# Optimization experiments

Hardware: AMD Instinct MI355X
Metric: run time of the kernel (lower is better)

The kernel has to match this reference:

```python
import jax, jax.numpy as jnp
import numpy as np

D_X, D_H, N_I = 1024, 64, 16  # model dim, per-head dim (d_q=d_k=d_v), heads
BSZ, SEQ = 2, 2048


def _linear(x, W, b):
    return x @ W.T + b


def setup_inputs() -> dict:
    key = jax.random.key(0)
    ks = jax.random.split(key, 16)
    s_in = 1.0 / np.sqrt(D_X)
    s_hd = 1.0 / np.sqrt(N_I * D_H)
    return {
        "query": jax.random.normal(ks[0], (BSZ, SEQ, D_X), jnp.float32),
        "key": jax.random.normal(ks[1], (BSZ, SEQ, D_X), jnp.float32),
        "value": jax.random.normal(ks[2], (BSZ, SEQ, D_X), jnp.float32),
        "Wq": jax.random.normal(ks[3], (N_I * D_H, D_X), jnp.float32) * s_in,
        "bq": jnp.zeros((N_I * D_H,), jnp.float32),
        "Wk": jax.random.normal(ks[4], (N_I * D_H, D_X), jnp.float32) * s_in,
        "bk": jnp.zeros((N_I * D_H,), jnp.float32),
        "Wv": jax.random.normal(ks[5], (N_I * D_H, D_X), jnp.float32) * s_in,
        "bv": jnp.zeros((N_I * D_H,), jnp.float32),
        "Wxv": jax.random.normal(ks[6], (N_I * D_H, D_X), jnp.float32) * s_in,
        "bxv": jnp.zeros((N_I * D_H,), jnp.float32),
        "Wxo": jax.random.normal(ks[7], (D_X, N_I * D_H), jnp.float32) * s_hd,
        "bxo": jnp.zeros((D_X,), jnp.float32),
        "Wmo": jax.random.normal(ks[8], (D_X, N_I * D_H), jnp.float32) * s_hd,
        "bmo": jnp.zeros((D_X,), jnp.float32),
    }


def reference(query, key, value, Wq, bq, Wk, bk, Wv, bv, Wxv, bxv, Wxo, bxo, Wmo, bmo):
    bsz, seq, _ = query.shape

    def heads(x):  # (b, s, n_I*d) -> (b, h, s, d)
        return x.reshape(bsz, seq, N_I, D_H).transpose(0, 2, 1, 3)

    Q = heads(_linear(query, Wq, bq))
    K = heads(_linear(key, Wk, bk))
    V = heads(_linear(value, Wv, bv))

    dot = jnp.einsum('bhid,bhjd->bhij', Q, K) / jnp.sqrt(jnp.float32(D_H))
    attention = jax.nn.softmax(dot, axis=-1)  # dropout p=0 (eval)

    # use_xv=True: replace K with xV = W_xv(key) for the k_bar aggregation
    xV = heads(_linear(key, Wxv, bxv))

    k_bar = jnp.einsum('bhjd,bhij->bhid', xV, attention)
    v_bar = jnp.einsum('bhjd,bhij->bhid', V, attention)

    def merge(x):  # (b, h, s, d) -> (b, s, h*d)
        return x.transpose(0, 2, 1, 3).reshape(bsz, seq, N_I * D_H)

    x = _linear(merge(k_bar), Wxo, bxo)
    m = _linear(merge(v_bar), Wmo, bmo)
    return (x, m)
```

## Files before the change

kernel.cpp:

```cpp
#include <hip/hip_runtime.h>
#include <math.h>

typedef __bf16 bf16;
typedef __bf16 bf16x2 __attribute__((ext_vector_type(2)));
typedef __bf16 bf16x4 __attribute__((ext_vector_type(4)));
typedef __bf16 bf16x8 __attribute__((ext_vector_type(8)));
typedef float f32x4 __attribute__((ext_vector_type(4)));

#define SEQ 2048
#define DH 64
#define DX 1024
#define NH 16
#define LP 72

static __device__ __forceinline__ f32x4 mfma16(bf16x8 a, bf16x8 b, f32x4 c) {
    return __builtin_amdgcn_mfma_f32_16x16x32_bf16(a, b, c, 0, 0, 0);
}
static __device__ __forceinline__ bf16x8 cvt8(const float* __restrict__ p) {
    f32x4 a = *(const f32x4*)p;
    f32x4 b = *(const f32x4*)(p + 4);
    bf16x8 r;
    #pragma unroll
    for (int j = 0; j < 4; ++j) { r[j] = (bf16)a[j]; r[4 + j] = (bf16)b[j]; }
    return r;
}

#define GL16(gp, lp) __builtin_amdgcn_global_load_lds( \
    (const __attribute__((address_space(1))) void*)(gp), \
    (__attribute__((address_space(3))) void*)(lp), 16, 0, 0)


__global__ __launch_bounds__(256) void cvt_all(
    const float* __restrict__ q, const float* __restrict__ k,
    const float* __restrict__ v,
    const float* __restrict__ w0, const float* __restrict__ w1,
    const float* __restrict__ w2, const float* __restrict__ w3,
    const float* __restrict__ w4, const float* __restrict__ w5,
    bf16* __restrict__ out)
{
    const size_t i = (size_t)blockIdx.x * 2048 + threadIdx.x * 8;
    const int seg = (int)(i >> 20);
    const float* s;
    size_t off;
    if (seg < 4)       { s = q; off = i; }
    else if (seg < 8)  { s = k; off = i - (4ull << 20); }
    else if (seg < 12) { s = v; off = i - (8ull << 20); }
    else {
        const float* ww[6] = {w0, w1, w2, w3, w4, w5};
        s = ww[seg - 12]; off = i - ((size_t)seg << 20);
    }
    *(bf16x8*)(out + i) = cvt8(s + off);
}

struct G4 {
    const bf16* X[4]; const bf16* W[4]; const float* B[4];
    bf16* Yb[4]; float* Yf[4]; int xmode[4]; int ymode[4];
};
__global__ __launch_bounds__(256) void gemm_fused(G4 a)
{
    __shared__ __align__(16) bf16 As[128 * 64];
    __shared__ __align__(16) bf16 Bs[128 * 64];

    const int z = blockIdx.z;
    const bf16* __restrict__ X = a.X[z];
    const bf16* __restrict__ W = a.W[z];
    const int xmode = a.xmode[z], ymode = a.ymode[z];

    const int tid  = threadIdx.x;
    const int wave = tid >> 6;
    const int lane = tid & 63;
    const int l16  = lane & 15;
    const int quad = lane >> 4;
    const int m0 = blockIdx.y * 128;
    const int n0 = blockIdx.x * 128;
    const int mw = (wave >> 1) * 64;
    const int nw = (wave & 1) * 64;

    const int srow = wave * 32 + (lane >> 3);
    const int scol = (lane & 7) * 8;

    f32x4 acc[4][4];
    #pragma unroll
    for (int i = 0; i < 4; ++i)
        #pragma unroll
        for (int j = 0; j < 4; ++j) acc[i][j] = (f32x4){0.f,0.f,0.f,0.f};

    for (int kb = 0; kb < DX / 64; ++kb) {
        __syncthreads();
        if (xmode == 0) {
            const bf16* ga = X + (size_t)(m0 + srow) * DX + kb * 64 + scol;
            #pragma unroll
            for (int j = 0; j < 4; ++j)
                GL16(ga + (size_t)j * 8 * DX, &As[(wave * 32 + j * 8) * 64]);
        } else {
            #pragma unroll
            for (int j = 0; j < 4; ++j) {
                const int m = m0 + srow + j * 8;
                const int b = m >> 11, s = m & 2047;
                GL16(X + ((size_t)(b * NH + kb) * SEQ + s) * DH + scol,
                     &As[(wave * 32 + j * 8) * 64]);
            }
        }
        {
            const bf16* gb = W + (size_t)(n0 + srow) * DX + kb * 64 + scol;
            #pragma unroll
            for (int j = 0; j < 4; ++j)
                GL16(gb + (size_t)j * 8 * DX, &Bs[(wave * 32 + j * 8) * 64]);
        }
        __syncthreads();

        #pragma unroll
        for (int ks = 0; ks < 2; ++ks) {
            bf16x8 af[4], bfr[4];
            #pragma unroll
            for (int mf = 0; mf < 4; ++mf)
                af[mf] = *(const bf16x8*)&As[(mw + mf * 16 + l16) * 64 + ks * 32 + quad * 8];
            #pragma unroll
            for (int nf = 0; nf < 4; ++nf)
                bfr[nf] = *(const bf16x8*)&Bs[(nw + nf * 16 + l16) * 64 + ks * 32 + quad * 8];
            #pragma unroll
            for (int mf = 0; mf < 4; ++mf)
                #pragma unroll
                for (int nf = 0; nf < 4; ++nf)
                    acc[mf][nf] = mfma16(af[mf], bfr[nf], acc[mf][nf]);
        }
    }

    #pragma unroll
    for (int nf = 0; nf < 4; ++nf) {
        const int col = n0 + nw + nf * 16 + l16;
        const float bvv = a.B[z][col];
        #pragma unroll
        for (int mf = 0; mf < 4; ++mf) {
            #pragma unroll
            for (int r = 0; r < 4; ++r) {
                const int row = m0 + mw + mf * 16 + quad * 4 + r;
                const float vv = acc[mf][nf][r] + bvv;
                if (ymode == 0) {
                    const int b = row >> 11, s = row & 2047;
                    const int h = col >> 6, d = col & 63;
                    a.Yb[z][((size_t)(b * NH + h) * SEQ + s) * DH + d] = (bf16)vv;
                } else {
                    a.Yf[z][(size_t)row * DX + col] = vv;
                }
            }
        }
    }
}

__global__ __launch_bounds__(256) void attn_fast(
    bf16* __restrict__ Q, const bf16* __restrict__ K,
    const bf16* __restrict__ V, const bf16* __restrict__ xV,
    bf16* __restrict__ VB)
{
    __shared__ __align__(16) bf16 Ks[2][64 * 64];
    __shared__ __align__(16) bf16 Vt [64 * LP];
    __shared__ __align__(16) bf16 xVt[64 * LP];
    __shared__ __align__(16) bf16 Pl[4][32 * LP];

    const int tid  = threadIdx.x;
    const int wave = tid >> 6;
    const int lane = tid & 63;
    const int l16  = lane & 15;
    const int quad = lane >> 4;
    const size_t hb = ((size_t)blockIdx.z * NH + blockIdx.y) * SEQ * DH;
    const int q0 = blockIdx.x * 128 + wave * 32;

    bf16x8 qf[2][2];
    #pragma unroll
    for (int mf = 0; mf < 2; ++mf)
        #pragma unroll
        for (int ks = 0; ks < 2; ++ks)
            qf[mf][ks] = *(const bf16x8*)(Q + hb + (size_t)(q0 + mf*16 + l16) * DH + ks*32 + quad*8);

    bf16x8 one8;
    #pragma unroll
    for (int j = 0; j < 8; ++j) one8[j] = (bf16)1.0f;

    f32x4 ov[2][4], oxv[2][4];
    f32x4 rsa[2];
    rsa[0] = (f32x4){0.f,0.f,0.f,0.f};
    rsa[1] = (f32x4){0.f,0.f,0.f,0.f};
    #pragma unroll
    for (int mf = 0; mf < 2; ++mf)
        #pragma unroll
        for (int c = 0; c < 4; ++c) {
            ov[mf][c]  = (f32x4){0.f,0.f,0.f,0.f};
            oxv[mf][c] = (f32x4){0.f,0.f,0.f,0.f};
        }

    const int krow = lane >> 3;
    const int kch  = (lane & 7) ^ krow;
    const int vkp = (tid & 31) * 2;
    const int vd0 = (tid >> 5) * 8;
    const float SCL = 0.125f * 1.4426950408889634f;

    bf16x8 pv0, pv1, px0, px1;
    {
        const bf16* kg = K + hb + (size_t)(wave*16 + krow) * DH + kch*8;
        GL16(kg,            &Ks[0][(wave*16 + 0) * 64]);
        GL16(kg + 8 * DH,   &Ks[0][(wave*16 + 8) * 64]);
        const size_t g0 = hb + (size_t)vkp * DH + vd0;
        pv0 = *(const bf16x8*)(V  + g0);
        pv1 = *(const bf16x8*)(V  + g0 + DH);
        px0 = *(const bf16x8*)(xV + g0);
        px1 = *(const bf16x8*)(xV + g0 + DH);
    }

    int c = 0;
    for (int kt = 0; kt < SEQ; kt += 64) {
        #pragma unroll
        for (int j = 0; j < 8; ++j) {
            *(bf16x2*)&Vt [(vd0 + j) * LP + vkp] = (bf16x2){pv0[j], pv1[j]};
            *(bf16x2*)&xVt[(vd0 + j) * LP + vkp] = (bf16x2){px0[j], px1[j]};
        }
        if (kt + 64 < SEQ) {
            const bf16* kg = K + hb + (size_t)(kt + 64 + wave*16 + krow) * DH + kch*8;
            GL16(kg,          &Ks[c ^ 1][(wave*16 + 0) * 64]);
            GL16(kg + 8 * DH, &Ks[c ^ 1][(wave*16 + 8) * 64]);
            const size_t g0 = hb + (size_t)(kt + 64 + vkp) * DH + vd0;
            pv0 = *(const bf16x8*)(V  + g0);
            pv1 = *(const bf16x8*)(V  + g0 + DH);
            px0 = *(const bf16x8*)(xV + g0);
            px1 = *(const bf16x8*)(xV + g0 + DH);
        }
        __asm__ volatile("s_waitcnt lgkmcnt(0)" ::: "memory");
        __builtin_amdgcn_s_barrier();
        __asm__ volatile("s_waitcnt vmcnt(6)" ::: "memory");
        __builtin_amdgcn_sched_barrier(0);

        f32x4 sf[4][2];
        #pragma unroll
        for (int mf = 0; mf < 4; ++mf)
            #pragma unroll
            for (int nf = 0; nf < 2; ++nf) sf[mf][nf] = (f32x4){0.f,0.f,0.f,0.f};
        __builtin_amdgcn_s_setprio(1);
        #pragma unroll
        for (int ks = 0; ks < 2; ++ks)
            #pragma unroll
            for (int mf = 0; mf < 4; ++mf) {
                bf16x8 kf = *(const bf16x8*)&Ks[c][(mf*16 + l16) * 64 +
                                                   (((ks*4 + quad) ^ (l16 & 7)) * 8)];
                sf[mf][0] = mfma16(kf, qf[0][ks], sf[mf][0]);
                sf[mf][1] = mfma16(kf, qf[1][ks], sf[mf][1]);
            }
        __builtin_amdgcn_s_setprio(0);

        #pragma unroll
        for (int nf = 0; nf < 2; ++nf)
            #pragma unroll
            for (int mf = 0; mf < 4; ++mf) {
                float p0 = __builtin_amdgcn_exp2f(sf[mf][nf][0] * SCL);
                float p1 = __builtin_amdgcn_exp2f(sf[mf][nf][1] * SCL);
                float p2 = __builtin_amdgcn_exp2f(sf[mf][nf][2] * SCL);
                float p3 = __builtin_amdgcn_exp2f(sf[mf][nf][3] * SCL);
                *(bf16x4*)&Pl[wave][(nf * 16 + l16) * LP + mf * 16 + quad * 4] =
                    (bf16x4){(bf16)p0, (bf16)p1, (bf16)p2, (bf16)p3};
            }
        __asm__ volatile("s_waitcnt lgkmcnt(0)" ::: "memory");
        __builtin_amdgcn_sched_barrier(0);

        __builtin_amdgcn_s_setprio(1);
        #pragma unroll
        for (int ks = 0; ks < 2; ++ks) {
            bf16x8 pa0 = *(const bf16x8*)&Pl[wave][(l16)      * LP + ks * 32 + quad * 8];
            bf16x8 pa1 = *(const bf16x8*)&Pl[wave][(16 + l16) * LP + ks * 32 + quad * 8];
            rsa[0] = mfma16(pa0, one8, rsa[0]);
            rsa[1] = mfma16(pa1, one8, rsa[1]);
            #pragma unroll
            for (int cc = 0; cc < 4; ++cc) {
                bf16x8 bv = *(const bf16x8*)&Vt [(cc * 16 + l16) * LP + ks * 32 + quad * 8];
                ov[0][cc]  = mfma16(pa0, bv, ov[0][cc]);
                ov[1][cc]  = mfma16(pa1, bv, ov[1][cc]);
                bf16x8 bx = *(const bf16x8*)&xVt[(cc * 16 + l16) * LP + ks * 32 + quad * 8];
                oxv[0][cc] = mfma16(pa0, bx, oxv[0][cc]);
                oxv[1][cc] = mfma16(pa1, bx, oxv[1][cc]);
            }
        }
        __builtin_amdgcn_s_setprio(0);

        __builtin_amdgcn_sched_barrier(0);
        __builtin_amdgcn_s_barrier();
        c ^= 1;
    }

    #pragma unroll
    for (int mf = 0; mf < 2; ++mf)
        #pragma unroll
        for (int r = 0; r < 4; ++r) {
            const int qrow = mf * 16 + quad * 4 + r;
            const float inv = 1.0f / rsa[mf][r];
            const size_t base = hb + (size_t)(q0 + qrow) * DH;
            #pragma unroll
            for (int cc = 0; cc < 4; ++cc) {
                const int d = cc * 16 + l16;
                Q [base + d] = (bf16)(oxv[mf][cc][r] * inv);
                VB[base + d] = (bf16)(ov[mf][cc][r]  * inv);
            }
        }
}


__global__ __launch_bounds__(256) void proj_gemm(
    const void* __restrict__ Xv, const float* __restrict__ W,
    const float* __restrict__ bias, void* __restrict__ Yv,
    int in_kind, int out_mode)
{
    __shared__ __align__(16) bf16 As[64 * LP];
    __shared__ __align__(16) bf16 Bs[128 * LP];
    const int tid  = threadIdx.x;
    const int wave = tid >> 6;
    const int lane = tid & 63;
    const int l16  = lane & 15;
    const int quad = lane >> 4;
    const int m0 = blockIdx.y * 64;
    const int n0 = blockIdx.x * 128;
    const int m_w = (wave >> 1) * 32;
    const int n_w = (wave & 1) * 64;
    const int ar = tid >> 2, ac = (tid & 3) * 16;
    const int br = tid >> 1, bc = (tid & 1) * 32;

    f32x4 acc[2][4];
    #pragma unroll
    for (int i = 0; i < 2; ++i)
        #pragma unroll
        for (int j = 0; j < 4; ++j) acc[i][j] = (f32x4){0.f,0.f,0.f,0.f};

    for (int kb = 0; kb < DX / 64; ++kb) {
        __syncthreads();
        if (in_kind == 0) {
            const float* xp = (const float*)Xv + (size_t)(m0 + ar) * DX + kb * 64 + ac;
            *(bf16x8*)&As[ar * LP + ac]     = cvt8(xp);
            *(bf16x8*)&As[ar * LP + ac + 8] = cvt8(xp + 8);
        } else {
            const bf16* xp = (const bf16*)Xv + ((size_t)kb * SEQ + (m0 + ar)) * DH + ac;
            *(bf16x8*)&As[ar * LP + ac]     = *(const bf16x8*)xp;
            *(bf16x8*)&As[ar * LP + ac + 8] = *(const bf16x8*)(xp + 8);
        }
        {
            const float* wp = W + (size_t)(n0 + br) * DX + kb * 64 + bc;
            #pragma unroll
            for (int g = 0; g < 4; ++g)
                *(bf16x8*)&Bs[br * LP + bc + g * 8] = cvt8(wp + g * 8);
        }
        __syncthreads();
        #pragma unroll
        for (int ks = 0; ks < 2; ++ks) {
            bf16x8 a0 = *(const bf16x8*)&As[(m_w + l16)      * LP + ks * 32 + quad * 8];
            bf16x8 a1 = *(const bf16x8*)&As[(m_w + 16 + l16) * LP + ks * 32 + quad * 8];
            #pragma unroll
            for (int nf = 0; nf < 4; ++nf) {
                bf16x8 b = *(const bf16x8*)&Bs[(n_w + nf * 16 + l16) * LP + ks * 32 + quad * 8];
                acc[0][nf] = mfma16(a0, b, acc[0][nf]);
                acc[1][nf] = mfma16(a1, b, acc[1][nf]);
            }
        }
    }
    #pragma unroll
    for (int mf = 0; mf < 2; ++mf)
        #pragma unroll
        for (int nf = 0; nf < 4; ++nf) {
            const int col = n0 + n_w + nf * 16 + l16;
            const float bvv = bias[col];
            #pragma unroll
            for (int r = 0; r < 4; ++r) {
                const int row = m0 + m_w + mf * 16 + quad * 4 + r;
                float v = acc[mf][nf][r] + bvv;
                if (out_mode == 0) {
                    int h = col >> 6, d = col & 63;
                    ((bf16*)Yv)[((size_t)h * SEQ + row) * DH + d] = (bf16)v;
                } else {
                    ((float*)Yv)[(size_t)row * DX + col] = v;
                }
            }
        }
}

__global__ __launch_bounds__(256) void attn_dual(
    bf16* __restrict__ Q, const bf16* __restrict__ K,
    const bf16* __restrict__ V, const bf16* __restrict__ xV,
    bf16* __restrict__ vb)
{
    __shared__ __align__(16) bf16 Ks [64 * LP];
    __shared__ __align__(16) bf16 Vt [64 * LP];
    __shared__ __align__(16) bf16 xVt[64 * LP];
    __shared__ __align__(16) bf16 Pl[4][32 * LP];
    const int tid  = threadIdx.x;
    const int h    = blockIdx.y;
    const int qt   = blockIdx.x;
    const int wave = tid >> 6;
    const int lane = tid & 63;
    const int l16  = lane & 15;
    const int quad = lane >> 4;
    const size_t hb = (size_t)h * SEQ * DH;
    const int q0 = qt * 128 + wave * 32;

    bf16x8 qf[2][2];
    #pragma unroll
    for (int mf = 0; mf < 2; ++mf)
        #pragma unroll
        for (int ks = 0; ks < 2; ++ks)
            qf[mf][ks] = *(const bf16x8*)(Q + hb + (size_t)(q0 + mf*16 + l16) * DH + ks*32 + quad*8);

    float mr[2][4], lr[2][4];
    f32x4 ov[2][4], oxv[2][4];
    #pragma unroll
    for (int mf = 0; mf < 2; ++mf)
        #pragma unroll
        for (int r = 0; r < 4; ++r) { mr[mf][r] = -1e30f; lr[mf][r] = 0.f; }
    #pragma unroll
    for (int mf = 0; mf < 2; ++mf)
        #pragma unroll
        for (int c = 0; c < 4; ++c) {
            ov[mf][c]  = (f32x4){0.f,0.f,0.f,0.f};
            oxv[mf][c] = (f32x4){0.f,0.f,0.f,0.f};
        }
    const int sr = tid >> 2, sc = (tid & 3) * 16;
    const int vkp = (tid & 31) * 2;
    const int vd0 = (tid >> 5) * 8;
    const float SCL = 0.125f * 1.4426950408889634f;

    for (int kt = 0; kt < SEQ; kt += 64) {
        __syncthreads();
        {
            const bf16* kpt = K + hb + (size_t)(kt + sr) * DH + sc;
            *(bf16x8*)&Ks[sr * LP + sc]     = *(const bf16x8*)kpt;
            *(bf16x8*)&Ks[sr * LP + sc + 8] = *(const bf16x8*)(kpt + 8);
            const size_t g0 = hb + (size_t)(kt + vkp) * DH + vd0;
            bf16x8 v0 = *(const bf16x8*)(V + g0);
            bf16x8 v1 = *(const bf16x8*)(V + g0 + DH);
            bf16x8 x0 = *(const bf16x8*)(xV + g0);
            bf16x8 x1 = *(const bf16x8*)(xV + g0 + DH);
            #pragma unroll
            for (int j = 0; j < 8; ++j) {
                *(bf16x2*)&Vt [(vd0 + j) * LP + vkp] = (bf16x2){v0[j], v1[j]};
                *(bf16x2*)&xVt[(vd0 + j) * LP + vkp] = (bf16x2){x0[j], x1[j]};
            }
        }
        __syncthreads();
        f32x4 sf[2][4];
        #pragma unroll
        for (int mf = 0; mf < 2; ++mf)
            #pragma unroll
            for (int nf = 0; nf < 4; ++nf) sf[mf][nf] = (f32x4){0.f,0.f,0.f,0.f};
        #pragma unroll
        for (int ks = 0; ks < 2; ++ks)
            #pragma unroll
            for (int nf = 0; nf < 4; ++nf) {
                bf16x8 bk = *(const bf16x8*)&Ks[(nf * 16 + l16) * LP + ks * 32 + quad * 8];
                sf[0][nf] = mfma16(qf[0][ks], bk, sf[0][nf]);
                sf[1][nf] = mfma16(qf[1][ks], bk, sf[1][nf]);
            }
        float mx[2][4], rs[2][4], alpha[2][4];
        #pragma unroll
        for (int mf = 0; mf < 2; ++mf)
            #pragma unroll
            for (int r = 0; r < 4; ++r) {
                float aa = fmaxf(sf[mf][0][r], sf[mf][1][r]);
                float bb = fmaxf(sf[mf][2][r], sf[mf][3][r]);
                mx[mf][r] = fmaxf(aa, bb) * SCL;
            }
        #pragma unroll
        for (int off = 1; off < 16; off <<= 1)
            #pragma unroll
            for (int mf = 0; mf < 2; ++mf)
                #pragma unroll
                for (int r = 0; r < 4; ++r)
                    mx[mf][r] = fmaxf(mx[mf][r], __shfl_xor(mx[mf][r], off, 64));
        #pragma unroll
        for (int mf = 0; mf < 2; ++mf)
            #pragma unroll
            for (int r = 0; r < 4; ++r) {
                float mnew = fmaxf(mr[mf][r], mx[mf][r]);
                alpha[mf][r] = exp2f(mr[mf][r] - mnew);
                mr[mf][r] = mnew;
            }
        bf16* pw = &Pl[wave][0];
        #pragma unroll
        for (int mf = 0; mf < 2; ++mf)
            #pragma unroll
            for (int r = 0; r < 4; ++r) rs[mf][r] = 0.f;
        #pragma unroll
        for (int mf = 0; mf < 2; ++mf)
            #pragma unroll
            for (int nf = 0; nf < 4; ++nf)
                #pragma unroll
                for (int r = 0; r < 4; ++r) {
                    float p = exp2f(sf[mf][nf][r] * SCL - mr[mf][r]);
                    rs[mf][r] += p;
                    pw[(mf * 16 + quad * 4 + r) * LP + nf * 16 + l16] = (bf16)p;
                }
        #pragma unroll
        for (int off = 1; off < 16; off <<= 1)
            #pragma unroll
            for (int mf = 0; mf < 2; ++mf)
                #pragma unroll
                for (int r = 0; r < 4; ++r)
                    rs[mf][r] += __shfl_xor(rs[mf][r], off, 64);
        #pragma unroll
        for (int mf = 0; mf < 2; ++mf)
            #pragma unroll
            for (int r = 0; r < 4; ++r)
                lr[mf][r] = lr[mf][r] * alpha[mf][r] + rs[mf][r];
        #pragma unroll
        for (int mf = 0; mf < 2; ++mf)
            #pragma unroll
            for (int c = 0; c < 4; ++c)
                #pragma unroll
                for (int r = 0; r < 4; ++r) {
                    ov[mf][c][r]  *= alpha[mf][r];
                    oxv[mf][c][r] *= alpha[mf][r];
                }
        __asm__ volatile("s_waitcnt lgkmcnt(0)" ::: "memory");
        #pragma unroll
        for (int ks = 0; ks < 2; ++ks) {
            bf16x8 pa0 = *(const bf16x8*)&Pl[wave][(l16)      * LP + ks * 32 + quad * 8];
            bf16x8 pa1 = *(const bf16x8*)&Pl[wave][(16 + l16) * LP + ks * 32 + quad * 8];
            #pragma unroll
            for (int c = 0; c < 4; ++c) {
                bf16x8 bv = *(const bf16x8*)&Vt [(c * 16 + l16) * LP + ks * 32 + quad * 8];
                ov[0][c]  = mfma16(pa0, bv, ov[0][c]);
                ov[1][c]  = mfma16(pa1, bv, ov[1][c]);
                bf16x8 bx = *(const bf16x8*)&xVt[(c * 16 + l16) * LP + ks * 32 + quad * 8];
                oxv[0][c] = mfma16(pa0, bx, oxv[0][c]);
                oxv[1][c] = mfma16(pa1, bx, oxv[1][c]);
            }
        }
    }
    #pragma unroll
    for (int mf = 0; mf < 2; ++mf)
        #pragma unroll
        for (int r = 0; r < 4; ++r) {
            const int s = q0 + mf * 16 + quad * 4 + r;
            const float inv = 1.0f / lr[mf][r];
            #pragma unroll
            for (int c = 0; c < 4; ++c) {
                const int d = c * 16 + l16;
                Q [hb + (size_t)s * DH + d] = (bf16)(oxv[mf][c][r] * inv);
                vb[hb + (size_t)s * DH + d] = (bf16)(ov[mf][c][r]  * inv);
            }
        }
}


extern "C" void kernel_launch(void* const* d_in, const int* in_sizes, int n_in,
                              void* d_out, int out_size, void* d_ws, size_t ws_size,
                              hipStream_t stream) {
    const float* query = (const float*)d_in[0];
    const float* key   = (const float*)d_in[1];
    const float* value = (const float*)d_in[2];
    const float* Wq  = (const float*)d_in[3];  const float* bq  = (const float*)d_in[4];
    const float* Wk  = (const float*)d_in[5];  const float* bk  = (const float*)d_in[6];
    const float* Wv  = (const float*)d_in[7];  const float* bv  = (const float*)d_in[8];
    const float* Wxv = (const float*)d_in[9];  const float* bxv = (const float*)d_in[10];
    const float* Wxo = (const float*)d_in[11]; const float* bxo = (const float*)d_in[12];
    const float* Wmo = (const float*)d_in[13]; const float* bmo = (const float*)d_in[14];

    float* out = (float*)d_out;
    const size_t SB = (size_t)SEQ * DX;
    const size_t M1 = 1ull << 20;

    dim3 blk(256);

    if (ws_size >= (76ull << 20)) {
        bf16* ws = (bf16*)d_ws;
        bf16* qb  = ws;
        bf16* kb  = ws + 4 * M1;
        bf16* vb  = ws + 8 * M1;
        bf16* Wqb = ws + 12 * M1;
        bf16* Wkb = Wqb + M1;
        bf16* Wvb = Wkb + M1;
        bf16* Wxvb= Wvb + M1;
        bf16* Wxob= Wxvb + M1;
        bf16* Wmob= Wxob + M1;
        bf16* Qs  = ws + 18 * M1;
        bf16* Kss = ws + 22 * M1;
        bf16* Vs  = ws + 26 * M1;
        bf16* xVs = ws + 30 * M1;
        bf16* VBs = ws + 34 * M1;

        cvt_all<<<9216, blk, 0, stream>>>(query, key, value,
                                          Wq, Wk, Wv, Wxv, Wxo, Wmo, ws + 0);

        G4 g1;
        g1.X[0]=qb;  g1.W[0]=Wqb;  g1.B[0]=bq;  g1.Yb[0]=Qs;  g1.Yf[0]=nullptr; g1.xmode[0]=0; g1.ymode[0]=0;
        g1.X[1]=kb;  g1.W[1]=Wkb;  g1.B[1]=bk;  g1.Yb[1]=Kss; g1.Yf[1]=nullptr; g1.xmode[1]=0; g1.ymode[1]=0;
        g1.X[2]=vb;  g1.W[2]=Wvb;  g1.B[2]=bv;  g1.Yb[2]=Vs;  g1.Yf[2]=nullptr; g1.xmode[2]=0; g1.ymode[2]=0;
        g1.X[3]=kb;  g1.W[3]=Wxvb; g1.B[3]=bxv; g1.Yb[3]=xVs; g1.Yf[3]=nullptr; g1.xmode[3]=0; g1.ymode[3]=0;
        gemm_fused<<<dim3(8, 32, 4), blk, 0, stream>>>(g1);

        attn_fast<<<dim3(16, NH, 2), blk, 0, stream>>>(Qs, Kss, Vs, xVs, VBs);

        G4 g2;
        g2.X[0]=Qs;  g2.W[0]=Wxob; g2.B[0]=bxo; g2.Yb[0]=nullptr; g2.Yf[0]=out;          g2.xmode[0]=1; g2.ymode[0]=1;
        g2.X[1]=VBs; g2.W[1]=Wmob; g2.B[1]=bmo; g2.Yb[1]=nullptr; g2.Yf[1]=out + 2*SB;   g2.xmode[1]=1; g2.ymode[1]=1;
        g2.X[2]=Qs;  g2.W[2]=Wxob; g2.B[2]=bxo; g2.Yb[2]=nullptr; g2.Yf[2]=out;          g2.xmode[2]=1; g2.ymode[2]=1;
        g2.X[3]=Qs;  g2.W[3]=Wxob; g2.B[3]=bxo; g2.Yb[3]=nullptr; g2.Yf[3]=out;          g2.xmode[3]=1; g2.ymode[3]=1;
        gemm_fused<<<dim3(8, 32, 2), blk, 0, stream>>>(g2);
    } else {
        bf16* Qs  = (bf16*)d_ws;
        bf16* Ksb = Qs  + SB;
        bf16* Vs  = Ksb + SB;
        bf16* xVs = Vs  + SB;
        bf16* vbs = xVs + SB;
        dim3 pg(8, 32);
        dim3 ag(16, NH);
        for (int b = 0; b < 2; ++b) {
            const float* q_b = query + (size_t)b * SB;
            const float* k_b = key   + (size_t)b * SB;
            const float* v_b = value + (size_t)b * SB;
            float* x_b = out + (size_t)b * SB;
            float* m_b = out + 2 * SB + (size_t)b * SB;
            proj_gemm<<<pg, blk, 0, stream>>>(q_b, Wq,  bq,  Qs,  0, 0);
            proj_gemm<<<pg, blk, 0, stream>>>(k_b, Wk,  bk,  Ksb, 0, 0);
            proj_gemm<<<pg, blk, 0, stream>>>(v_b, Wv,  bv,  Vs,  0, 0);
            proj_gemm<<<pg, blk, 0, stream>>>(k_b, Wxv, bxv, xVs, 0, 0);
            attn_dual<<<ag, blk, 0, stream>>>(Qs, Ksb, Vs, xVs, vbs);
            proj_gemm<<<pg, blk, 0, stream>>>(Qs,  Wxo, bxo, x_b, 1, 1);
            proj_gemm<<<pg, blk, 0, stream>>>(vbs, Wmo, bmo, m_b, 1, 1);
        }
    }
}
```

Baseline: 303.2 us.

## Replace projection GEMM with larger-tile double-buffered swizzled 512-thread kernel

The 128x128 fused projection GEMM is replaced by a templated kernel with 256-wide N tiles (BM=256 for the input projections, BM=128 for the output projections), 8 waves per block, double-buffered LDS staging that prefetches the next K-block while computing the current one, and an XOR swizzle on LDS columns to avoid bank conflicts. The aim is more operand reuse per global load, overlap of load latency with MFMA work, and fewer LDS conflicts. In exchange it uses more LDS and more accumulator registers, which may lower occupancy, and the smaller grid (256 or 256 blocks) may fill the CUs less evenly.

Result: faster. 290.9 us (-4.0%).

```diff
diff --git a/kernel.cpp b/kernel.cpp
--- a/kernel.cpp
+++ b/kernel.cpp
@@ -56,10 +56,13 @@
     const bf16* X[4]; const bf16* W[4]; const float* B[4];
     bf16* Yb[4]; float* Yf[4]; int xmode[4]; int ymode[4];
 };
-__global__ __launch_bounds__(256) void gemm_fused(G4 a)
+
+template<int BM>
+__global__ __launch_bounds__(512) void gemm256(G4 a)
 {
-    __shared__ __align__(16) bf16 As[128 * 64];
-    __shared__ __align__(16) bf16 Bs[128 * 64];
+    constexpr int MREP = BM / 32;
+    __shared__ __align__(16) bf16 As[2][BM * 64];
+    __shared__ __align__(16) bf16 Bs[2][256 * 64];
 
     const int z = blockIdx.z;
     const bf16* __restrict__ X = a.X[z];
@@ -67,74 +70,81 @@
     const int xmode = a.xmode[z], ymode = a.ymode[z];
 
     const int tid  = threadIdx.x;
-    const int wave = tid >> 6;
+    const int wid  = tid >> 6;
     const int lane = tid & 63;
     const int l16  = lane & 15;
     const int quad = lane >> 4;
-    const int m0 = blockIdx.y * 128;
-    const int n0 = blockIdx.x * 128;
-    const int mw = (wave >> 1) * 64;
-    const int nw = (wave & 1) * 64;
-
-    const int srow = wave * 32 + (lane >> 3);
-    const int scol = (lane & 7) * 8;
-
-    f32x4 acc[4][4];
-    #pragma unroll
-    for (int i = 0; i < 4; ++i)
+    const int wm   = wid >> 2;
+    const int wn   = wid & 3;
+    const int m0 = blockIdx.y * BM;
+    const int n0 = blockIdx.x * 256;
+
+    const int srow8 = lane >> 3;
+    const int sch   = (lane & 7) ^ srow8;
+
+    f32x4 acc[MREP][4];
+    #pragma unroll
+    for (int i = 0; i < MREP; ++i)
         #pragma unroll
         for (int j = 0; j < 4; ++j) acc[i][j] = (f32x4){0.f,0.f,0.f,0.f};
 
+    auto stage = [&](int buf, int kb) {
+        #pragma unroll
+        for (int g = 0; g < BM / 64; ++g) {
+            const int row = g * 64 + wid * 8 + srow8;
+            const bf16* src;
+            if (xmode == 0) {
+                src = X + (size_t)(m0 + row) * DX + kb * 64 + sch * 8;
+            } else {
+                const int m = m0 + row;
+                const int b = m >> 11, s = m & 2047;
+                src = X + ((size_t)(b * NH + kb) * SEQ + s) * DH + sch * 8;
+            }
+            GL16(src, &As[buf][(g * 64 + wid * 8) * 64]);
+        }
+        #pragma unroll
+        for (int g = 0; g < 4; ++g) {
+            const int row = g * 64 + wid * 8 + srow8;
+            const bf16* src = W + (size_t)(n0 + row) * DX + kb * 64 + sch * 8;
+            GL16(src, &Bs[buf][(g * 64 + wid * 8) * 64]);
+        }
+    };
+
+    stage(0, 0);
+    __syncthreads();
+
+    int cur = 0;
     for (int kb = 0; kb < DX / 64; ++kb) {
-        __syncthreads();
-        if (xmode == 0) {
-            const bf16* ga = X + (size_t)(m0 + srow) * DX + kb * 64 + scol;
-            #pragma unroll
-            for (int j = 0; j < 4; ++j)
-                GL16(ga + (size_t)j * 8 * DX, &As[(wave * 32 + j * 8) * 64]);
-        } else {
-            #pragma unroll
-            for (int j = 0; j < 4; ++j) {
-                const int m = m0 + srow + j * 8;
-                const int b = m >> 11, s = m & 2047;
-                GL16(X + ((size_t)(b * NH + kb) * SEQ + s) * DH + scol,
-                     &As[(wave * 32 + j * 8) * 64]);
-            }
-        }
-        {
-            const bf16* gb = W + (size_t)(n0 + srow) * DX + kb * 64 + scol;
-            #pragma unroll
-            for (int j = 0; j < 4; ++j)
-                GL16(gb + (size_t)j * 8 * DX, &Bs[(wave * 32 + j * 8) * 64]);
-        }
-        __syncthreads();
-
+        if (kb + 1 < DX / 64) stage(cur ^ 1, kb + 1);
         #pragma unroll
         for (int ks = 0; ks < 2; ++ks) {
-            bf16x8 af[4], bfr[4];
-            #pragma unroll
-            for (int mf = 0; mf < 4; ++mf)
-                af[mf] = *(const bf16x8*)&As[(mw + mf * 16 + l16) * 64 + ks * 32 + quad * 8];
+            bf16x8 af[MREP], bfr[4];
+            const int cc = (ks * 4 + quad) ^ (l16 & 7);
+            #pragma unroll
+            for (int mf = 0; mf < MREP; ++mf)
+                af[mf] = *(const bf16x8*)&As[cur][(wm * (BM/2) + mf * 16 + l16) * 64 + cc * 8];
             #pragma unroll
             for (int nf = 0; nf < 4; ++nf)
-                bfr[nf] = *(const bf16x8*)&Bs[(nw + nf * 16 + l16) * 64 + ks * 32 + quad * 8];
-            #pragma unroll
-            for (int mf = 0; mf < 4; ++mf)
+                bfr[nf] = *(const bf16x8*)&Bs[cur][(wn * 64 + nf * 16 + l16) * 64 + cc * 8];
+            #pragma unroll
+            for (int mf = 0; mf < MREP; ++mf)
                 #pragma unroll
                 for (int nf = 0; nf < 4; ++nf)
                     acc[mf][nf] = mfma16(af[mf], bfr[nf], acc[mf][nf]);
         }
+        __syncthreads();
+        cur ^= 1;
     }
 
     #pragma unroll
     for (int nf = 0; nf < 4; ++nf) {
-        const int col = n0 + nw + nf * 16 + l16;
+        const int col = n0 + wn * 64 + nf * 16 + l16;
         const float bvv = a.B[z][col];
         #pragma unroll
-        for (int mf = 0; mf < 4; ++mf) {
+        for (int mf = 0; mf < MREP; ++mf) {
             #pragma unroll
             for (int r = 0; r < 4; ++r) {
-                const int row = m0 + mw + mf * 16 + quad * 4 + r;
+                const int row = m0 + wm * (BM/2) + mf * 16 + quad * 4 + r;
                 const float vv = acc[mf][nf][r] + bvv;
                 if (ymode == 0) {
                     const int b = row >> 11, s = row & 2047;
@@ -587,7 +597,7 @@
         g1.X[1]=kb;  g1.W[1]=Wkb;  g1.B[1]=bk;  g1.Yb[1]=Kss; g1.Yf[1]=nullptr; g1.xmode[1]=0; g1.ymode[1]=0;
         g1.X[2]=vb;  g1.W[2]=Wvb;  g1.B[2]=bv;  g1.Yb[2]=Vs;  g1.Yf[2]=nullptr; g1.xmode[2]=0; g1.ymode[2]=0;
         g1.X[3]=kb;  g1.W[3]=Wxvb; g1.B[3]=bxv; g1.Yb[3]=xVs; g1.Yf[3]=nullptr; g1.xmode[3]=0; g1.ymode[3]=0;
-        gemm_fused<<<dim3(8, 32, 4), blk, 0, stream>>>(g1);
+        gemm256<256><<<dim3(4, 16, 4), dim3(512), 0, stream>>>(g1);
 
         attn_fast<<<dim3(16, NH, 2), blk, 0, stream>>>(Qs, Kss, Vs, xVs, VBs);
 
@@ -596,7 +606,7 @@
         g2.X[1]=VBs; g2.W[1]=Wmob; g2.B[1]=bmo; g2.Yb[1]=nullptr; g2.Yf[1]=out + 2*SB;   g2.xmode[1]=1; g2.ymode[1]=1;
         g2.X[2]=Qs;  g2.W[2]=Wxob; g2.B[2]=bxo; g2.Yb[2]=nullptr; g2.Yf[2]=out;          g2.xmode[2]=1; g2.ymode[2]=1;
         g2.X[3]=Qs;  g2.W[3]=Wxob; g2.B[3]=bxo; g2.Yb[3]=nullptr; g2.Yf[3]=out;          g2.xmode[3]=1; g2.ymode[3]=1;
-        gemm_fused<<<dim3(8, 32, 2), blk, 0, stream>>>(g2);
+        gemm256<128><<<dim3(4, 32, 2), dim3(512), 0, stream>>>(g2);
     } else {
         bf16* Qs  = (bf16*)d_ws;
         bf16* Ksb = Qs  + SB;
```
